# Optimization experiments

Hardware: AMD Instinct MI355X
Metric: run time of the kernel (lower is better)

Reference implementation:

```python
import jax, jax.numpy as jnp
import numpy as np
from jax import lax

EPS = 1e-5

def setup_inputs() -> dict:
    key = jax.random.key(0)
    k1, k2, k3 = jax.random.split(key, 3)
    B, S, D, W = 4, 4096, 2048, 4
    x = jax.random.normal(k1, (B, S, D), dtype=jnp.float32)
    norm_weight = jnp.ones((D,), dtype=jnp.float32)
    conv_weight = jax.random.normal(k2, (D, W), dtype=jnp.float32) * (1.0 / np.sqrt(W))
    proj_weight = jax.random.normal(k3, (2, D), dtype=jnp.float32) * (1.0 / np.sqrt(D))
    return {"x": x, "norm_weight": norm_weight, "conv_weight": conv_weight, "proj_weight": proj_weight}

def _rmsnorm(x, w):
    var = jnp.mean(x * x, axis=-1, keepdims=True)
    return x * lax.rsqrt(var + EPS) * w

def _causal_dw_conv_silu(h, conv_weight):
    # h: [B,S,D], conv_weight: [D,W]; causal depthwise conv along seq + silu
    B, S, D = h.shape
    W = conv_weight.shape[-1]
    hc = jnp.transpose(h, (0, 2, 1))                      # [B,D,S]
    hc = jnp.pad(hc, ((0, 0), (0, 0), (W - 1, 0)))        # left-pad for causality
    y = lax.conv_general_dilated(
        hc, conv_weight[:, None, :], window_strides=(1,), padding='VALID',
        dimension_numbers=('NCH', 'OIH', 'NCH'), feature_group_count=D)
    return jnp.transpose(jax.nn.silu(y), (0, 2, 1))       # [B,S,D]

def reference(x, norm_weight, conv_weight, proj_weight):
    B, S, D = x.shape
    h = _rmsnorm(x, norm_weight)
    h = _causal_dw_conv_silu(h, conv_weight)
    logits = jnp.einsum('bsd,od->bso', h, proj_weight)    # [B,S,2]
    gate = jax.nn.softmax(logits, axis=-1)[..., 1]        # [B,S]
    mask = gate > 0.5                                     # [B,S]
    # cumsum-index scatter-compress: selected tokens packed to the front,
    # unselected tokens routed to slot 0 which is dropped (padded to S, vs
    # data-dependent max_q in torch).
    idx = jnp.where(mask, jnp.cumsum(mask.astype(jnp.int32), axis=1), 0)  # [B,S]
    buf = jnp.zeros((B, S + 1, D), dtype=x.dtype)
    bidx = jnp.arange(B)[:, None]
    buf = buf.at[bidx, idx].set(x)
    return buf[:, 1:]
```

## Files before the change

kernel.cpp:

```cpp
#include <hip/hip_runtime.h>
#include <cstddef>

#define BATCH 4
#define SEQ   4096
#define DIM   2048
#define EPSF  1e-5f
#define TCHUNK 8
#define CPB   (SEQ / TCHUNK)
#define NBLK  (BATCH * CPB)

__device__ __forceinline__ float wave_sum(float v) {
#pragma unroll
    for (int off = 32; off > 0; off >>= 1)
        v += __shfl_down(v, off, 64);
    return v;
}

__global__ __launch_bounds__(256, 3) void mask_kernel(
    const float* __restrict__ x, const float* __restrict__ nw,
    const float* __restrict__ cw, const float* __restrict__ pw,
    unsigned short* __restrict__ tok)
{
    __shared__ float lds_ss[3][4][4];
    __shared__ float lds_acc[2][4][4];

    const int t = threadIdx.x, lane = t & 63, wid = t >> 6;
    const int G = gridDim.x;
    const int chunk = (blockIdx.x & 7) * (G >> 3) + (blockIdx.x >> 3);
    const int b  = chunk / CPB;
    const int s0 = (chunk % CPB) * TCHUNK;
    const int d0 = 4 * t, d1 = d0 + 1024;

    float cwn[8][4], pd[8];
    {
        float4 n0 = *(const float4*)(nw + d0);
        float4 n1 = *(const float4*)(nw + d1);
        float nv[8] = {n0.x, n0.y, n0.z, n0.w, n1.x, n1.y, n1.z, n1.w};
#pragma unroll
        for (int i = 0; i < 8; ++i) {
            const int d = (i < 4) ? (d0 + i) : (d1 + i - 4);
            float4 c4 = *(const float4*)(cw + 4 * d);
            cwn[i][0] = c4.x * nv[i]; cwn[i][1] = c4.y * nv[i];
            cwn[i][2] = c4.z * nv[i]; cwn[i][3] = c4.w * nv[i];
        }
        float4 a0 = *(const float4*)(pw + d0);
        float4 a1 = *(const float4*)(pw + d1);
        float4 b0 = *(const float4*)(pw + DIM + d0);
        float4 b1 = *(const float4*)(pw + DIM + d1);
        pd[0] = b0.x - a0.x; pd[1] = b0.y - a0.y; pd[2] = b0.z - a0.z; pd[3] = b0.w - a0.w;
        pd[4] = b1.x - a1.x; pd[5] = b1.y - a1.y; pd[6] = b1.z - a1.z; pd[7] = b1.w - a1.w;
    }

    const float* xb = x + (size_t)b * SEQ * DIM;
    float h1[8], h2[8], h3[8];

    {
        float wv[3][8];
#pragma unroll
        for (int w = 0; w < 3; ++w) {
            const int s = s0 - 3 + w;
            if (s >= 0) {
                float4 a = *(const float4*)(xb + (size_t)s * DIM + d0);
                float4 c = *(const float4*)(xb + (size_t)s * DIM + d1);
                wv[w][0]=a.x; wv[w][1]=a.y; wv[w][2]=a.z; wv[w][3]=a.w;
                wv[w][4]=c.x; wv[w][5]=c.y; wv[w][6]=c.z; wv[w][7]=c.w;
            } else {
#pragma unroll
                for (int i = 0; i < 8; ++i) wv[w][i] = 0.f;
            }
            float ss = 0.f;
#pragma unroll
            for (int i = 0; i < 8; ++i) ss += wv[w][i] * wv[w][i];
            ss = wave_sum(ss);
            if (lane == 0) lds_ss[2][w][wid] = ss;
        }
        __syncthreads();
#pragma unroll
        for (int w = 0; w < 3; ++w) {
            const float sum4 = lds_ss[2][w][0] + lds_ss[2][w][1]
                             + lds_ss[2][w][2] + lds_ss[2][w][3];
            const float rstd = 1.0f / sqrtf(sum4 * (1.0f / DIM) + EPSF);
            float* h = (w == 0) ? h3 : (w == 1) ? h2 : h1;
#pragma unroll
            for (int i = 0; i < 8; ++i) h[i] = wv[w][i] * rstd;
        }
    }

    int pending = -1;
#pragma unroll
    for (int g = 0; g < 2; ++g) {
        float xv[4][8];
#pragma unroll
        for (int j = 0; j < 4; ++j) {
            const int s = s0 + 4 * g + j;
            float4 a = *(const float4*)(xb + (size_t)s * DIM + d0);
            float4 c = *(const float4*)(xb + (size_t)s * DIM + d1);
            xv[j][0]=a.x; xv[j][1]=a.y; xv[j][2]=a.z; xv[j][3]=a.w;
            xv[j][4]=c.x; xv[j][5]=c.y; xv[j][6]=c.z; xv[j][7]=c.w;
        }
#pragma unroll
        for (int j = 0; j < 4; ++j) {
            float ss = 0.f;
#pragma unroll
            for (int i = 0; i < 8; ++i) ss += xv[j][i] * xv[j][i];
            ss = wave_sum(ss);
            if (lane == 0) lds_ss[g][j][wid] = ss;
        }
        __syncthreads();
        if (pending >= 0 && t < 4) {
            const float a = lds_acc[pending][t][0] + lds_acc[pending][t][1]
                          + lds_acc[pending][t][2] + lds_acc[pending][t][3];
            tok[b * SEQ + s0 + 4 * pending + t] = (a > 0.f) ? 0x8000 : 0;
        }
#pragma unroll
        for (int j = 0; j < 4; ++j) {
            const float sum4 = lds_ss[g][j][0] + lds_ss[g][j][1]
                             + lds_ss[g][j][2] + lds_ss[g][j][3];
            const float rstd = 1.0f / sqrtf(sum4 * (1.0f / DIM) + EPSF);
            float acc = 0.f;
#pragma unroll
            for (int i = 0; i < 8; ++i) {
                const float hc = xv[j][i] * rstd;
                const float y = cwn[i][0] * h3[i] + cwn[i][1] * h2[i]
                              + cwn[i][2] * h1[i] + cwn[i][3] * hc;
                const float sig = 1.0f / (1.0f + __expf(-y));
                acc += (y * sig) * pd[i];
                h3[i] = h2[i]; h2[i] = h1[i]; h1[i] = hc;
            }
            acc = wave_sum(acc);
            if (lane == 0) lds_acc[g][j][wid] = acc;
        }
        pending = g;
    }
    __syncthreads();
    if (t < 4) {
        const float a = lds_acc[1][t][0] + lds_acc[1][t][1]
                      + lds_acc[1][t][2] + lds_acc[1][t][3];
        tok[b * SEQ + s0 + 4 + t] = (a > 0.f) ? 0x8000 : 0;
    }
}

__global__ __launch_bounds__(256) void scan_kernel(unsigned short* __restrict__ tok)
{
    const int b = blockIdx.x, t = threadIdx.x;
    const int PER = SEQ / 256;
    __shared__ int wtot[4];

    int m[PER], tot = 0;
#pragma unroll
    for (int i = 0; i < PER; ++i) {
        m[i] = tok[b * SEQ + t * PER + i] >> 15;
        tot += m[i];
    }
    const int lane = t & 63, wid = t >> 6;
    int inc = tot;
#pragma unroll
    for (int off = 1; off < 64; off <<= 1) {
        int v = __shfl_up(inc, off, 64);
        if (lane >= off) inc += v;
    }
    if (lane == 63) wtot[wid] = inc;
    __syncthreads();
    int pref = inc - tot;
    for (int w = 0; w < wid; ++w) pref += wtot[w];

    int run = pref;
#pragma unroll
    for (int i = 0; i < PER; ++i) {
        run += m[i];
        tok[b * SEQ + t * PER + i] = (unsigned short)((m[i] << 15) | run);
    }
}

__global__ __launch_bounds__(256) void scatter_kernel(
    const float* __restrict__ x, const unsigned short* __restrict__ tok,
    float* __restrict__ out)
{
    const int b = blockIdx.x / SEQ;
    const int s = blockIdx.x - b * SEQ;
    const int t = threadIdx.x;
    const unsigned v    = tok[b * SEQ + s];
    const int     nsel  = tok[b * SEQ + SEQ - 1] & 0x7FFF;
    const int     p     = v & 0x7FFF;
    const int     dest  = (v & 0x8000u) ? (p - 1) : (nsel + s - p);
    float* o = out + ((size_t)b * SEQ + dest) * DIM;
    if (v & 0x8000u) {
        const float* src = x + ((size_t)b * SEQ + s) * DIM;
        *(float4*)(o + 4 * t)        = *(const float4*)(src + 4 * t);
        *(float4*)(o + 4 * t + 1024) = *(const float4*)(src + 4 * t + 1024);
    } else {
        const float4 z = make_float4(0.f, 0.f, 0.f, 0.f);
        *(float4*)(o + 4 * t)        = z;
        *(float4*)(o + 4 * t + 1024) = z;
    }
}

extern "C" void kernel_launch(void* const* d_in, const int* in_sizes, int n_in,
                              void* d_out, int out_size, void* d_ws, size_t ws_size,
                              hipStream_t stream) {
    const float* x  = (const float*)d_in[0];
    const float* nw = (const float*)d_in[1];
    const float* cw = (const float*)d_in[2];
    const float* pw = (const float*)d_in[3];
    float* out = (float*)d_out;

    unsigned short* tok = (unsigned short*)d_ws;

    mask_kernel<<<NBLK, 256, 0, stream>>>(x, nw, cw, pw, tok);
    scan_kernel<<<BATCH, 256, 0, stream>>>(tok);
    scatter_kernel<<<BATCH * SEQ, 256, 0, stream>>>(x, tok, out);
}
```

Baseline: 264.2 us.

## Fuse mask, scan and scatter via decoupled look-back single-pass compaction

Merges the mask, scan and scatter kernels into one compaction kernel. Blocks take chunks in order from an atomic ticket and compute per-chunk counts, then find their global offset with a decoupled look-back over a status array. Each block writes its selected rows straight to the output while the x rows are still fresh, which avoids a second full read of x. A separate kernel zeroes only the tail rows past the selected count. The cost is a memset, a spin-wait that serialises prefix propagation across chunks, and lower occupancy (launch bounds 2 instead of 3).

```diff
diff --git a/kernel.cpp b/kernel.cpp
--- a/kernel.cpp
+++ b/kernel.cpp
@@ -5,9 +5,13 @@
 #define SEQ   4096
 #define DIM   2048
 #define EPSF  1e-5f
-#define TCHUNK 8
-#define CPB   (SEQ / TCHUNK)
-#define NBLK  (BATCH * CPB)
+#define TCH   8
+#define CPB   (SEQ / TCH)
+#define NCHUNK (BATCH * CPB)
+
+#define F_AGG 0x40000000u
+#define F_INC 0x80000000u
+#define CMASK 0xFFFFu
 
 __device__ __forceinline__ float wave_sum(float v) {
 #pragma unroll
@@ -15,20 +19,31 @@
         v += __shfl_down(v, off, 64);
     return v;
 }
-
-__global__ __launch_bounds__(256, 3) void mask_kernel(
+__device__ __forceinline__ int wave_sum_i(int v) {
+#pragma unroll
+    for (int off = 32; off > 0; off >>= 1)
+        v += __shfl_down(v, off, 64);
+    return v;
+}
+
+__global__ __launch_bounds__(256, 2) void compact_kernel(
     const float* __restrict__ x, const float* __restrict__ nw,
     const float* __restrict__ cw, const float* __restrict__ pw,
-    unsigned short* __restrict__ tok)
+    unsigned* __restrict__ status, unsigned* __restrict__ ticket,
+    int* __restrict__ nsel, float* __restrict__ out)
 {
     __shared__ float lds_ss[3][4][4];
-    __shared__ float lds_acc[2][4][4];
+    __shared__ float lds_acc[8][4];
+    __shared__ int   lds_excl;
+    __shared__ unsigned lds_ch;
 
     const int t = threadIdx.x, lane = t & 63, wid = t >> 6;
-    const int G = gridDim.x;
-    const int chunk = (blockIdx.x & 7) * (G >> 3) + (blockIdx.x >> 3);
-    const int b  = chunk / CPB;
-    const int s0 = (chunk % CPB) * TCHUNK;
+    if (t == 0) lds_ch = atomicAdd(ticket, 1u);
+    __syncthreads();
+    const int ch = (int)lds_ch;
+    const int b  = ch & 3;
+    const int c  = ch >> 2;
+    const int s0 = c * TCH;
     const int d0 = 4 * t, d1 = d0 + 1024;
 
     float cwn[8][4], pd[8];
@@ -61,9 +76,9 @@
             const int s = s0 - 3 + w;
             if (s >= 0) {
                 float4 a = *(const float4*)(xb + (size_t)s * DIM + d0);
-                float4 c = *(const float4*)(xb + (size_t)s * DIM + d1);
+                float4 cc = *(const float4*)(xb + (size_t)s * DIM + d1);
                 wv[w][0]=a.x; wv[w][1]=a.y; wv[w][2]=a.z; wv[w][3]=a.w;
-                wv[w][4]=c.x; wv[w][5]=c.y; wv[w][6]=c.z; wv[w][7]=c.w;
+                wv[w][4]=cc.x; wv[w][5]=cc.y; wv[w][6]=cc.z; wv[w][7]=cc.w;
             } else {
 #pragma unroll
                 for (int i = 0; i < 8; ++i) wv[w][i] = 0.f;
@@ -86,7 +101,6 @@
         }
     }
 
-    int pending = -1;
 #pragma unroll
     for (int g = 0; g < 2; ++g) {
         float xv[4][8];
@@ -94,9 +108,9 @@
         for (int j = 0; j < 4; ++j) {
             const int s = s0 + 4 * g + j;
             float4 a = *(const float4*)(xb + (size_t)s * DIM + d0);
-            float4 c = *(const float4*)(xb + (size_t)s * DIM + d1);
+            float4 cc = *(const float4*)(xb + (size_t)s * DIM + d1);
             xv[j][0]=a.x; xv[j][1]=a.y; xv[j][2]=a.z; xv[j][3]=a.w;
-            xv[j][4]=c.x; xv[j][5]=c.y; xv[j][6]=c.z; xv[j][7]=c.w;
+            xv[j][4]=cc.x; xv[j][5]=cc.y; xv[j][6]=cc.z; xv[j][7]=cc.w;
         }
 #pragma unroll
         for (int j = 0; j < 4; ++j) {
@@ -107,11 +121,6 @@
             if (lane == 0) lds_ss[g][j][wid] = ss;
         }
         __syncthreads();
-        if (pending >= 0 && t < 4) {
-            const float a = lds_acc[pending][t][0] + lds_acc[pending][t][1]
-                          + lds_acc[pending][t][2] + lds_acc[pending][t][3];
-            tok[b * SEQ + s0 + 4 * pending + t] = (a > 0.f) ? 0x8000 : 0;
-        }
 #pragma unroll
         for (int j = 0; j < 4; ++j) {
             const float sum4 = lds_ss[g][j][0] + lds_ss[g][j][1]
@@ -128,71 +137,80 @@
                 h3[i] = h2[i]; h2[i] = h1[i]; h1[i] = hc;
             }
             acc = wave_sum(acc);
-            if (lane == 0) lds_acc[g][j][wid] = acc;
-        }
-        pending = g;
+            if (lane == 0) lds_acc[4 * g + j][wid] = acc;
+        }
     }
     __syncthreads();
-    if (t < 4) {
-        const float a = lds_acc[1][t][0] + lds_acc[1][t][1]
-                      + lds_acc[1][t][2] + lds_acc[1][t][3];
-        tok[b * SEQ + s0 + 4 + t] = (a > 0.f) ? 0x8000 : 0;
-    }
-}
-
-__global__ __launch_bounds__(256) void scan_kernel(unsigned short* __restrict__ tok)
-{
-    const int b = blockIdx.x, t = threadIdx.x;
-    const int PER = SEQ / 256;
-    __shared__ int wtot[4];
-
-    int m[PER], tot = 0;
-#pragma unroll
-    for (int i = 0; i < PER; ++i) {
-        m[i] = tok[b * SEQ + t * PER + i] >> 15;
-        tot += m[i];
-    }
-    const int lane = t & 63, wid = t >> 6;
-    int inc = tot;
-#pragma unroll
-    for (int off = 1; off < 64; off <<= 1) {
-        int v = __shfl_up(inc, off, 64);
-        if (lane >= off) inc += v;
-    }
-    if (lane == 63) wtot[wid] = inc;
+
+    int m[8], pfx[8], agg = 0;
+#pragma unroll
+    for (int j = 0; j < 8; ++j) {
+        const float a = lds_acc[j][0] + lds_acc[j][1]
+                      + lds_acc[j][2] + lds_acc[j][3];
+        m[j] = (a > 0.f) ? 1 : 0;
+        pfx[j] = agg;
+        agg += m[j];
+    }
+
+    if (t == 0)
+        __hip_atomic_store(&status[ch], F_AGG | (unsigned)agg,
+                           __ATOMIC_RELEASE, __HIP_MEMORY_SCOPE_AGENT);
+    if (wid == 0) {
+        int excl = 0;
+        int look = c - 1;
+        while (look >= 0) {
+            const int pos = look - lane;
+            unsigned st = F_INC;
+            if (pos >= 0)
+                st = __hip_atomic_load(&status[(pos << 2) | b],
+                                       __ATOMIC_RELAXED, __HIP_MEMORY_SCOPE_AGENT);
+            const unsigned long long mi = __ballot((st & F_INC) != 0);
+            const unsigned long long ma = __ballot((st & (F_AGG | F_INC)) != 0);
+            if (mi) {
+                const int L = (int)(__ffsll((long long)mi) - 1);
+                if (L == 0 || ((~ma) & ((1ULL << L) - 1)) == 0) {
+                    int cnt = (lane <= L) ? (int)(st & CMASK) : 0;
+                    excl += wave_sum_i(cnt);
+                    break;
+                }
+            } else if (~ma == 0ULL) {
+                excl += wave_sum_i((int)(st & CMASK));
+                look -= 64;
+                continue;
+            }
+            __builtin_amdgcn_s_sleep(2);
+        }
+        if (lane == 0) {
+            lds_excl = excl;
+            __hip_atomic_store(&status[ch], F_INC | (unsigned)(excl + agg),
+                               __ATOMIC_RELEASE, __HIP_MEMORY_SCOPE_AGENT);
+            if (c == CPB - 1) nsel[b] = excl + agg;
+        }
+    }
     __syncthreads();
-    int pref = inc - tot;
-    for (int w = 0; w < wid; ++w) pref += wtot[w];
-
-    int run = pref;
-#pragma unroll
-    for (int i = 0; i < PER; ++i) {
-        run += m[i];
-        tok[b * SEQ + t * PER + i] = (unsigned short)((m[i] << 15) | run);
-    }
-}
-
-__global__ __launch_bounds__(256) void scatter_kernel(
-    const float* __restrict__ x, const unsigned short* __restrict__ tok,
-    float* __restrict__ out)
+    const int excl = lds_excl;
+
+#pragma unroll
+    for (int j = 0; j < 8; ++j) {
+        if (m[j]) {
+            const float* src = xb + (size_t)(s0 + j) * DIM;
+            float* o = out + ((size_t)b * SEQ + (excl + pfx[j])) * DIM;
+            *(float4*)(o + d0) = *(const float4*)(src + d0);
+            *(float4*)(o + d1) = *(const float4*)(src + d1);
+        }
+    }
+}
+
+__global__ __launch_bounds__(256) void tail_zero_kernel(
+    const int* __restrict__ nsel, float* __restrict__ out)
 {
     const int b = blockIdx.x / SEQ;
-    const int s = blockIdx.x - b * SEQ;
-    const int t = threadIdx.x;
-    const unsigned v    = tok[b * SEQ + s];
-    const int     nsel  = tok[b * SEQ + SEQ - 1] & 0x7FFF;
-    const int     p     = v & 0x7FFF;
-    const int     dest  = (v & 0x8000u) ? (p - 1) : (nsel + s - p);
-    float* o = out + ((size_t)b * SEQ + dest) * DIM;
-    if (v & 0x8000u) {
-        const float* src = x + ((size_t)b * SEQ + s) * DIM;
-        *(float4*)(o + 4 * t)        = *(const float4*)(src + 4 * t);
-        *(float4*)(o + 4 * t + 1024) = *(const float4*)(src + 4 * t + 1024);
-    } else {
-        const float4 z = make_float4(0.f, 0.f, 0.f, 0.f);
-        *(float4*)(o + 4 * t)        = z;
-        *(float4*)(o + 4 * t + 1024) = z;
-    }
+    const int r = blockIdx.x - b * SEQ;
+    if (r < nsel[b]) return;
+    float* o = out + ((size_t)b * SEQ + r) * DIM;
+    const float4 z = make_float4(0.f, 0.f, 0.f, 0.f);
+    *(float4*)(o + 4 * threadIdx.x)        = z;
+    *(float4*)(o + 4 * threadIdx.x + 1024) = z;
 }
 
 extern "C" void kernel_launch(void* const* d_in, const int* in_sizes, int n_in,
@@ -204,9 +222,11 @@
     const float* pw = (const float*)d_in[3];
     float* out = (float*)d_out;
 
-    unsigned short* tok = (unsigned short*)d_ws;
-
-    mask_kernel<<<NBLK, 256, 0, stream>>>(x, nw, cw, pw, tok);
-    scan_kernel<<<BATCH, 256, 0, stream>>>(tok);
-    scatter_kernel<<<BATCH * SEQ, 256, 0, stream>>>(x, tok, out);
-}
+    unsigned* status = (unsigned*)d_ws;
+    unsigned* ticket = status + NCHUNK;
+    int*      nsel   = (int*)(status + NCHUNK + 4);
+
+    hipMemsetAsync(d_ws, 0, (NCHUNK + 8) * sizeof(unsigned), stream);
+    compact_kernel<<<NCHUNK, 256, 0, stream>>>(x, nw, cw, pw, status, ticket, nsel, out);
+    tail_zero_kernel<<<BATCH * SEQ, 256, 0, stream>>>(nsel, out);
+}
```

New measurement: 399.9 us. 1.51x slower.
